# Performance work log

Hardware: AMD Instinct MI355X
Metric: run time of the kernel (lower is better)

The kernel has to match this reference:

```python
import jax, jax.numpy as jnp
import numpy as np

# --- fan-beam (flat detector) FBP geometry constants, matching init geo dict ---
V, U = 720, 736            # sino_views, nDetecU
NX = NY = 512              # nVoxelX, nVoxelY
SVOX = 400.0               # sVoxelX = sVoxelY (mm)
DU = 1.2858                # dDetecU (mm)
DSO, DOD = 595.0, 490.6    # source-origin, origin-detector distances
DSD = DSO + DOD
DBETA = 2.0 * np.pi / V    # angular step (full 2*pi scan, endpoint=False)


def _ramp_filter_fft():
    """Ram-Lak ramp filter (Kak & Slaney discrete spatial kernel), FFT'd for fast conv."""
    n = np.arange(-(U - 1), U)
    h = np.zeros(2 * U - 1, np.float64)
    h[U - 1] = 1.0 / (4.0 * DU * DU)
    odd = (np.abs(n) % 2 == 1)
    h[odd] = -1.0 / (np.pi * n[odd] * DU) ** 2
    L = int(2 ** np.ceil(np.log2(2 * (2 * U - 1))))  # zero-pad length (linear conv)
    return jnp.asarray(np.fft.fft(h, L).astype(np.complex64)), L

_HF, _L = _ramp_filter_fft()


def setup_inputs() -> dict:
    key = jax.random.key(0)
    sinogram = jax.random.uniform(key, (1, 1, V, U), dtype=jnp.float32)
    return {"sinogram": sinogram}


def reference(sinogram):
    # --- 1) cosine weighting of each detector sample ---
    sino = sinogram.reshape(V, U)
    us = (jnp.arange(U, dtype=jnp.float32) - (U - 1) / 2.0) * DU  # detector coords
    sino_w = sino * (DSD / jnp.sqrt(DSD * DSD + us * us))

    # --- 2) Ram-Lak ramp filtering per view (FFT linear convolution) ---
    Qf = jnp.fft.ifft(jnp.fft.fft(sino_w, n=_L, axis=1) * _HF[None, :], axis=1)
    Q = (jnp.real(Qf)[:, U - 1:2 * U - 1] * DU).astype(jnp.float32)  # [V, U]

    # --- 3) weighted fan-beam backprojection (scan over angles, O(Nx*Ny) carry) ---
    dx = SVOX / NX
    xs = (jnp.arange(NX, dtype=jnp.float32) - (NX - 1) / 2.0) * dx
    X, Y = jnp.meshgrid(xs, xs, indexing='ij')  # [NX, NY]
    betas = jnp.linspace(0.0, 2.0 * np.pi, V, endpoint=False).astype(jnp.float32)

    def body(img, ang_q):
        beta, q = ang_q                       # q: filtered projection [U]
        cb, sb = jnp.cos(beta), jnp.sin(beta)
        t = X * cb + Y * sb                   # coord along detector direction
        s = -X * sb + Y * cb                  # coord toward source
        D = DSO - s                           # source-to-pixel axial distance
        u = DSD * t / D                       # flat-detector intersection (mm)
        idx = u / DU + (U - 1) / 2.0          # fractional detector index
        i0 = jnp.clip(jnp.floor(idx), 0, U - 2).astype(jnp.int32)
        f = idx - i0
        val = q[i0] * (1.0 - f) + q[i0 + 1] * f
        val = jnp.where((idx >= 0.0) & (idx <= U - 1.0), val, 0.0)
        return img + (DSO / D) ** 2 * val, None

    img0 = jnp.zeros((NX, NY), jnp.float32)
    img, _ = jax.lax.scan(body, img0, (betas, Q))
    # 0.5 factor: full 2*pi fan scan covers each ray twice
    return (img * (0.5 * DBETA)).reshape(1, 1, NX, NY)
```

## Files before the change

### kernel.cpp

```cpp
#include <hip/hip_runtime.h>
#include <math.h>

#define NV 720
#define NU 736
#define NUP 768
#define NXY 512

__global__ __launch_bounds__(512) void filter_kernel(const float* __restrict__ sino,
                                                     float* __restrict__ Q,
                                                     float4* __restrict__ trig,
                                                     float* __restrict__ out_zero) {
    __shared__ float s4[2][368][4];
    __shared__ float wco[736];
    __shared__ float part[3][128][8];
    const int bx = blockIdx.x;
    const int q = bx & 3;
    const int vb = bx >> 2;
    const int v0 = vb * 4;
    const int tid = threadIdx.x;
    const int tz = tid >> 7;
    const int J0 = tid & 127;

    for (int i = bx * 512 + tid; i < NXY * NXY; i += 720 * 512)
        out_zero[i] = 0.0f;

    if (q == 0 && tid < 4) {
        int v = v0 + tid;
        float beta = (float)((double)v * (2.0 * M_PI / 720.0));
        float cb = cosf(beta), sb = sinf(beta);
        const float K = (float)(1085.6 / 1.2858);
        trig[v] = make_float4(cb * K, sb * K, cb, sb);
    }
    const float DSD2 = (float)(1085.6 * 1085.6);
    for (int i = tid; i < 4 * NU; i += 512) {
        const int vv = i / NU, u = i - vv * NU;
        float us = ((float)u - 367.5f) * 1.2858f;
        float cw = 1085.6f / sqrtf(DSD2 + us * us);
        s4[u & 1][u >> 1][vv] = sino[(v0 + vv) * NU + u] * cw;
    }
    for (int i = tid; i < 736; i += 512) {
        double n = (double)(2 * i - 735);
        double a = M_PI * n * 1.2858;
        wco[i] = (float)(-1.0 / (a * a));
    }
    __syncthreads();

    const int m0 = 92 * tz;
    float a00 = 0.f, a01 = 0.f, a02 = 0.f, a03 = 0.f;
    float a10 = 0.f, a11 = 0.f, a12 = 0.f, a13 = 0.f;
    const int J0c = min(J0, 91);
    const int y0 = J0c + 367 + 92 * q;
    const float* wp = &wco[y0 - m0];

    #pragma unroll 4
    for (int mm = 0; mm < 92; ++mm) {
        const int m = m0 + mm;
        const float w0 = wp[-mm];
        const float w1 = wp[1 - mm];
        const float4 sv1 = *(const float4*)&s4[1][m][0];
        const float4 sv0 = *(const float4*)&s4[0][m][0];
        a00 = fmaf(w0, sv1.x, a00); a01 = fmaf(w0, sv1.y, a01);
        a02 = fmaf(w0, sv1.z, a02); a03 = fmaf(w0, sv1.w, a03);
        a10 = fmaf(w1, sv0.x, a10); a11 = fmaf(w1, sv0.y, a11);
        a12 = fmaf(w1, sv0.z, a12); a13 = fmaf(w1, sv0.w, a13);
    }

    if (tz != 0 && J0 < 92) {
        *(float4*)&part[tz - 1][J0][0] = make_float4(a00, a01, a02, a03);
        *(float4*)&part[tz - 1][J0][4] = make_float4(a10, a11, a12, a13);
    }
    __syncthreads();

    if (tz == 0 && J0 < 92) {
        #pragma unroll
        for (int g = 0; g < 3; ++g) {
            const float4 p0 = *(const float4*)&part[g][J0][0];
            const float4 p1 = *(const float4*)&part[g][J0][4];
            a00 += p0.x; a01 += p0.y; a02 += p0.z; a03 += p0.w;
            a10 += p1.x; a11 += p1.y; a12 += p1.z; a13 += p1.w;
        }
        const float H0 = (float)(1.0 / (4.0 * 1.2858 * 1.2858));
        const int mc = J0 + 92 * q;
        const float4 c0 = *(const float4*)&s4[0][mc][0];
        const float4 c1 = *(const float4*)&s4[1][mc][0];
        a00 = fmaf(H0, c0.x, a00); a01 = fmaf(H0, c0.y, a01);
        a02 = fmaf(H0, c0.z, a02); a03 = fmaf(H0, c0.w, a03);
        a10 = fmaf(H0, c1.x, a10); a11 = fmaf(H0, c1.y, a11);
        a12 = fmaf(H0, c1.z, a12); a13 = fmaf(H0, c1.w, a13);
        const int j0i = 2 * mc;
        const float DU = 1.2858f;
        *(float2*)&Q[(v0 + 0) * NUP + j0i] = make_float2(a00 * DU, a10 * DU);
        *(float2*)&Q[(v0 + 1) * NUP + j0i] = make_float2(a01 * DU, a11 * DU);
        *(float2*)&Q[(v0 + 2) * NUP + j0i] = make_float2(a02 * DU, a12 * DU);
        *(float2*)&Q[(v0 + 3) * NUP + j0i] = make_float2(a03 * DU, a13 * DU);
    }
}

__global__ __launch_bounds__(256) void bp_kernel(const float* __restrict__ Q,
                                                 const float4* __restrict__ trig,
                                                 float* __restrict__ out) {
    __shared__ float win[2][4][NUP];
    const int b = blockIdx.x;
    const int c = b & 15;
    const int blk = b >> 4;
    const int bx = blk >> 4;
    const int by = blk & 15;
    const int t = threadIdx.x;
    const int w = t >> 6;
    const int l = t & 63;
    const int iq = (bx << 4) + ((w >> 1) << 3) + (l >> 3);
    const int jq = (by << 4) + ((w & 1) << 3) + (l & 7);

    const float dx = 400.0f / 512.0f;
    const float X = ((float)iq - 255.5f) * dx;
    const float Y = ((float)jq - 255.5f) * dx;
    const float Kc = (float)(1085.6 / 1.2858);

    float acc0 = 0.0f, acc1 = 0.0f, acc2 = 0.0f, acc3 = 0.0f;
    const bool inr = fmaf(X, X, Y * Y) <= 236.5f * 236.5f;
    const bool myint = __all(inr);

    const int nk = (c < 4) ? 12 : 11;
    const float* rowp = Q + (size_t)(c + 180 * w) * NUP;
    const float4* tvp = trig + c;

    #pragma unroll
    for (int ch = 0; ch < 3; ++ch)
        __builtin_amdgcn_global_load_lds(
            (const __attribute__((address_space(1))) void*)(rowp + ch * 256 + l * 4),
            (__attribute__((address_space(3))) void*)&win[0][w][ch * 256],
            16, 0, 0);

    for (int it = 0; it < nk; ++it) {
        __syncthreads();
        if (it + 1 < nk) {
            const float* rn = rowp + 16 * NUP;
            #pragma unroll
            for (int ch = 0; ch < 3; ++ch)
                __builtin_amdgcn_global_load_lds(
                    (const __attribute__((address_space(1))) void*)(rn + ch * 256 + l * 4),
                    (__attribute__((address_space(3))) void*)&win[(it + 1) & 1][w][ch * 256],
                    16, 0, 0);
        }
        const float* winf = &win[it & 1][0][0];

        __builtin_amdgcn_s_setprio(1);
        if (myint) {
            const float4 tv = tvp[0];
            float a = fmaf(tv.z, X, tv.w * Y);
            float bb = fmaf(tv.z, Y, -tv.w * X);
            float aK = a * Kc, bK = bb * Kc;
            float D0 = 595.0f - bb, D1 = 595.0f + a, D2 = 595.0f + bb, D3 = 595.0f - a;
            float r0 = __builtin_amdgcn_rcpf(D0);
            float r1 = __builtin_amdgcn_rcpf(D1);
            float r2 = __builtin_amdgcn_rcpf(D2);
            float r3 = __builtin_amdgcn_rcpf(D3);
            float fi0 = fmaf(aK,  r0, 367.5f);
            float fi1 = fmaf(bK,  r1, 367.5f);
            float fi2 = fmaf(-aK, r2, 367.5f);
            float fi3 = fmaf(-bK, r3, 367.5f);
            int im[4] = {(int)fi0, (int)fi1, (int)fi2, (int)fi3};
            float ff[4] = {__builtin_amdgcn_fractf(fi0), __builtin_amdgcn_fractf(fi1),
                           __builtin_amdgcn_fractf(fi2), __builtin_amdgcn_fractf(fi3)};
            float gg[4] = {r0 * r0, r1 * r1, r2 * r2, r3 * r3};
            float* accp[4] = {&acc0, &acc1, &acc2, &acc3};
            #pragma unroll
            for (int m = 0; m < 4; ++m) {
                #pragma unroll
                for (int k = 0; k < 4; ++k) {
                    const float* p = winf + (k * NUP + im[m]);
                    float q0 = p[0];
                    float q1 = p[1];
                    float val = fmaf(ff[m], q1 - q0, q0);
                    *accp[(m - k) & 3] = fmaf(gg[m], val, *accp[(m - k) & 3]);
                }
            }
        } else {
            const float4 tvs[4] = {tvp[0], tvp[180], tvp[360], tvp[540]};
            const float pX[4] = {X, Y, -X, -Y};
            const float pY[4] = {Y, -X, -Y, X};
            float* accp[4] = {&acc0, &acc1, &acc2, &acc3};
            #pragma unroll
            for (int j = 0; j < 4; ++j) {
                float Xm = pX[j], Ym = pY[j];
                #pragma unroll
                for (int k = 0; k < 4; ++k) {
                    const float4 tv = tvs[k];
                    float t2 = fmaf(tv.x, Xm, tv.y * Ym);
                    float D  = fmaf(tv.w, Xm, fmaf(tv.z, -Ym, 595.0f));
                    float rD = __builtin_amdgcn_rcpf(D);
                    float fidx = fmaf(t2, rD, 367.5f);
                    int i0c = min(max((int)fidx, 0), NU - 2);
                    float f = __builtin_amdgcn_fractf(fidx);
                    const float* p = winf + (k * NUP + i0c);
                    float q0 = p[0];
                    float q1 = p[1];
                    float val = fmaf(f, q1 - q0, q0);
                    float cen = fidx - 367.5f;
                    float g = (__builtin_fabsf(cen) <= 367.5f) ? rD * rD : 0.0f;
                    *accp[j] = fmaf(g, val, *accp[j]);
                }
            }
        }
        __builtin_amdgcn_s_setprio(0);
        rowp += 16 * NUP;
        tvp += 16;
    }
    const float SC = (float)(595.0 * 595.0 * 0.5 * (2.0 * M_PI / 720.0));
    const int ir = 511 - iq, jr = 511 - jq;
    unsafeAtomicAdd(&out[iq * NXY + jq], acc0 * SC);
    unsafeAtomicAdd(&out[jq * NXY + ir], acc1 * SC);
    unsafeAtomicAdd(&out[ir * NXY + jr], acc2 * SC);
    unsafeAtomicAdd(&out[jr * NXY + iq], acc3 * SC);
}

extern "C" void kernel_launch(void* const* d_in, const int* in_sizes, int n_in,
                              void* d_out, int out_size, void* d_ws, size_t ws_size,
                              hipStream_t stream) {
    const float* sino = (const float*)d_in[0];
    float* out = (float*)d_out;
    float* Q = (float*)d_ws;
    float4* trig = (float4*)((char*)d_ws + (size_t)NV * NUP * sizeof(float));

    filter_kernel<<<720, 512, 0, stream>>>(sino, Q, trig, out);
    bp_kernel<<<4096, 256, 0, stream>>>(Q, trig, out);
}
```

Baseline: 113.0 us.

## Interleave the four symmetric views per detector bin in the filtered projection buffer

The filter kernel now writes Q in an interleaved layout where the four views separated by 90 degrees (v, v+180, v+360, v+540) sit next to each other for each detector bin. The backprojection kernel loads these contiguous 3072-float rows into shared memory and reads the four views' samples at im*4+k instead of from four separate rows. The intent is that the symmetric-pixel gathers in the inner loop hit nearby LDS addresses, so they can be merged into wider reads with fewer bank conflicts. In exchange, the filter kernel's global stores become scattered strided scalar writes instead of float2 writes.

```diff
diff --git a/kernel.cpp b/kernel.cpp
--- a/kernel.cpp
+++ b/kernel.cpp
@@ -7,7 +7,7 @@
 #define NXY 512
 
 __global__ __launch_bounds__(512) void filter_kernel(const float* __restrict__ sino,
-                                                     float* __restrict__ Q,
+                                                     float* __restrict__ Qi,
                                                      float4* __restrict__ trig,
                                                      float* __restrict__ out_zero) {
     __shared__ float s4[2][368][4];
@@ -89,14 +89,17 @@
         a12 = fmaf(H0, c1.z, a12); a13 = fmaf(H0, c1.w, a13);
         const int j0i = 2 * mc;
         const float DU = 1.2858f;
-        *(float2*)&Q[(v0 + 0) * NUP + j0i] = make_float2(a00 * DU, a10 * DU);
-        *(float2*)&Q[(v0 + 1) * NUP + j0i] = make_float2(a01 * DU, a11 * DU);
-        *(float2*)&Q[(v0 + 2) * NUP + j0i] = make_float2(a02 * DU, a12 * DU);
-        *(float2*)&Q[(v0 + 3) * NUP + j0i] = make_float2(a03 * DU, a13 * DU);
+        const int v180 = v0 % 180;
+        const int wq = v0 / 180;
+        float* qr = Qi + (size_t)v180 * 3072 + wq;
+        qr[0 * 3072 + 4 * j0i]       = a00 * DU;  qr[0 * 3072 + 4 * (j0i + 1)] = a10 * DU;
+        qr[1 * 3072 + 4 * j0i]       = a01 * DU;  qr[1 * 3072 + 4 * (j0i + 1)] = a11 * DU;
+        qr[2 * 3072 + 4 * j0i]       = a02 * DU;  qr[2 * 3072 + 4 * (j0i + 1)] = a12 * DU;
+        qr[3 * 3072 + 4 * j0i]       = a03 * DU;  qr[3 * 3072 + 4 * (j0i + 1)] = a13 * DU;
     }
 }
 
-__global__ __launch_bounds__(256) void bp_kernel(const float* __restrict__ Q,
+__global__ __launch_bounds__(256) void bp_kernel(const float* __restrict__ Qi,
                                                  const float4* __restrict__ trig,
                                                  float* __restrict__ out) {
     __shared__ float win[2][4][NUP];
@@ -121,24 +124,24 @@
     const bool myint = __all(inr);
 
     const int nk = (c < 4) ? 12 : 11;
-    const float* rowp = Q + (size_t)(c + 180 * w) * NUP;
+    const float* rowp = Qi + (size_t)c * 3072;
     const float4* tvp = trig + c;
 
     #pragma unroll
     for (int ch = 0; ch < 3; ++ch)
         __builtin_amdgcn_global_load_lds(
-            (const __attribute__((address_space(1))) void*)(rowp + ch * 256 + l * 4),
+            (const __attribute__((address_space(1))) void*)(rowp + w * 768 + ch * 256 + l * 4),
             (__attribute__((address_space(3))) void*)&win[0][w][ch * 256],
             16, 0, 0);
 
     for (int it = 0; it < nk; ++it) {
         __syncthreads();
         if (it + 1 < nk) {
-            const float* rn = rowp + 16 * NUP;
+            const float* rn = rowp + 16 * 3072;
             #pragma unroll
             for (int ch = 0; ch < 3; ++ch)
                 __builtin_amdgcn_global_load_lds(
-                    (const __attribute__((address_space(1))) void*)(rn + ch * 256 + l * 4),
+                    (const __attribute__((address_space(1))) void*)(rn + w * 768 + ch * 256 + l * 4),
                     (__attribute__((address_space(3))) void*)&win[(it + 1) & 1][w][ch * 256],
                     16, 0, 0);
         }
@@ -166,11 +169,11 @@
             float* accp[4] = {&acc0, &acc1, &acc2, &acc3};
             #pragma unroll
             for (int m = 0; m < 4; ++m) {
+                const float* pm = winf + 4 * im[m];
                 #pragma unroll
                 for (int k = 0; k < 4; ++k) {
-                    const float* p = winf + (k * NUP + im[m]);
-                    float q0 = p[0];
-                    float q1 = p[1];
+                    float q0 = pm[k];
+                    float q1 = pm[k + 4];
                     float val = fmaf(ff[m], q1 - q0, q0);
                     *accp[(m - k) & 3] = fmaf(gg[m], val, *accp[(m - k) & 3]);
                 }
@@ -192,9 +195,9 @@
                     float fidx = fmaf(t2, rD, 367.5f);
                     int i0c = min(max((int)fidx, 0), NU - 2);
                     float f = __builtin_amdgcn_fractf(fidx);
-                    const float* p = winf + (k * NUP + i0c);
-                    float q0 = p[0];
-                    float q1 = p[1];
+                    const float* pe = winf + 4 * i0c;
+                    float q0 = pe[k];
+                    float q1 = pe[k + 4];
                     float val = fmaf(f, q1 - q0, q0);
                     float cen = fidx - 367.5f;
                     float g = (__builtin_fabsf(cen) <= 367.5f) ? rD * rD : 0.0f;
@@ -203,7 +206,7 @@
             }
         }
         __builtin_amdgcn_s_setprio(0);
-        rowp += 16 * NUP;
+        rowp += 16 * 3072;
         tvp += 16;
     }
     const float SC = (float)(595.0 * 595.0 * 0.5 * (2.0 * M_PI / 720.0));
@@ -219,9 +222,9 @@
                               hipStream_t stream) {
     const float* sino = (const float*)d_in[0];
     float* out = (float*)d_out;
-    float* Q = (float*)d_ws;
-    float4* trig = (float4*)((char*)d_ws + (size_t)NV * NUP * sizeof(float));
-
-    filter_kernel<<<720, 512, 0, stream>>>(sino, Q, trig, out);
-    bp_kernel<<<4096, 256, 0, stream>>>(Q, trig, out);
+    float* Qi = (float*)d_ws;
+    float4* trig = (float4*)((char*)d_ws + (size_t)180 * 3072 * sizeof(float));
+
+    filter_kernel<<<720, 512, 0, stream>>>(sino, Qi, trig, out);
+    bp_kernel<<<4096, 256, 0, stream>>>(Qi, trig, out);
 }
```

After: 108.3 us. -4.1%, faster.
